# Kernel tuning notes

Hardware: AMD Instinct MI355X
Metric: run time of the kernel (lower is better)

## Reference

```python
import jax, jax.numpy as jnp
import numpy as np

NEG_SLOPE = 0.2  # PyG GATConv default negative_slope
N_NODES = 50000


def gat_conv(x, src, dst, W, att_src, att_dst, bias, heads, out_ch):
    # x: [N, F_in]; src/dst: [E] (messages flow src -> dst, softmax over dst)
    N = x.shape[0]
    h = (x @ W).reshape(N, heads, out_ch)              # [N,H,C]
    a_src = jnp.sum(h * att_src, axis=-1)              # [N,H]
    a_dst = jnp.sum(h * att_dst, axis=-1)              # [N,H]
    e = jax.nn.leaky_relu(a_src[src] + a_dst[dst], NEG_SLOPE)   # [E,H]
    # numerically stable segment softmax over incoming edges of each dst node
    m = jax.ops.segment_max(e, dst, num_segments=N)    # [N,H]
    e = jnp.exp(e - m[dst])
    denom = jax.ops.segment_sum(e, dst, num_segments=N)
    alpha = e / (denom[dst] + 1e-16)                   # [E,H]
    msg = h[src] * alpha[:, :, None]                   # [E,H,C]
    out = jax.ops.segment_sum(msg, dst, num_segments=N)  # [N,H,C]
    return out.reshape(N, heads * out_ch) + bias


def add_self_loops(edge_index, num_nodes):
    loop = jnp.arange(num_nodes, dtype=edge_index.dtype)
    return jnp.concatenate([edge_index, jnp.stack([loop, loop])], axis=1)


def setup_inputs() -> dict:
    key = jax.random.key(0)
    ks = jax.random.split(key, 10)
    F_in, H, C, F_out = 256, 4, 64, 16
    x = jax.random.normal(ks[0], (N_NODES, F_in), dtype=jnp.float32)
    edge_index = jax.random.randint(ks[1], (2, 800000), 0, N_NODES, dtype=jnp.int64)
    s1 = 1.0 / np.sqrt(F_in)
    s2 = 1.0 / np.sqrt(H * C)
    return {
        "x": x,
        "edge_index": edge_index,
        "W1": jax.random.normal(ks[2], (F_in, H * C), dtype=jnp.float32) * s1,
        "att_src1": jax.random.normal(ks[3], (H, C), dtype=jnp.float32) * s2,
        "att_dst1": jax.random.normal(ks[4], (H, C), dtype=jnp.float32) * s2,
        "b1": jnp.zeros((H * C,), dtype=jnp.float32),
        "W2": jax.random.normal(ks[5], (H * C, F_out), dtype=jnp.float32) * s2,
        "att_src2": jax.random.normal(ks[6], (1, F_out), dtype=jnp.float32) * 0.25,
        "att_dst2": jax.random.normal(ks[7], (1, F_out), dtype=jnp.float32) * 0.25,
        "b2": jnp.zeros((F_out,), dtype=jnp.float32),
    }


def reference(x, edge_index, W1, att_src1, att_dst1, b1, W2, att_src2, att_dst2, b2):
    ei = add_self_loops(edge_index, x.shape[0])
    src, dst = ei[0], ei[1]
    H1, C1 = att_src1.shape
    h = gat_conv(x, src, dst, W1, att_src1, att_dst1, b1, H1, C1)
    h = jax.nn.relu(h)
    # F.dropout(training=False) is identity in eval mode
    H2, C2 = att_src2.shape
    out = gat_conv(h, src, dst, W2, att_src2, att_dst2, b2, H2, C2)
    return jax.nn.log_softmax(out, axis=1)
```

## Files before the change

### kernel.cpp

```cpp
#include <hip/hip_runtime.h>
#include <math.h>


typedef __attribute__((ext_vector_type(8))) short bf16x8;
typedef __attribute__((ext_vector_type(8))) unsigned short u16x8;
typedef __attribute__((ext_vector_type(4))) float f32x4;
typedef __attribute__((ext_vector_type(2))) float f32x2;

static __device__ inline unsigned short f2bf(float f) {
    unsigned u = __builtin_bit_cast(unsigned, f);
    unsigned r = (u + 0x7FFF + ((u >> 16) & 1)) >> 16;
    return (unsigned short)r;
}
static __device__ inline float bf2f(unsigned short u) {
    unsigned v = ((unsigned)u) << 16;
    return __builtin_bit_cast(float, v);
}
static __device__ inline float lrelu(float x) { return x > 0.f ? x : 0.2f * x; }

__global__ __launch_bounds__(256) void k_prep(const float* __restrict__ W1,
                                              const float* __restrict__ b1,
                                              const float* __restrict__ W2,
                                              short* __restrict__ w1t,
                                              float* __restrict__ b1p,
                                              float* __restrict__ w2p,
                                              int* __restrict__ cnt,
                                              float* __restrict__ a1s,
                                              float* __restrict__ a2s,
                                              unsigned* __restrict__ h1f8u,
                                              float* __restrict__ h2,
                                              int N) {
    int idx = blockIdx.x * 256 + threadIdx.x;
    if (idx < N) cnt[idx] = 0;
    if (idx < 256) {
        int ct = (idx >> 6) * 64 + (idx & 3) * 16 + ((idx & 63) >> 2);
        b1p[idx] = b1[ct];
    }
    if (idx < 4096) {
        int pp = idx >> 4, c2 = idx & 15;
        int ct = (pp >> 6) * 64 + (pp & 3) * 16 + ((pp & 63) >> 2);
        w2p[idx] = W2[ct * 16 + c2];
    }
    if (idx < 4) a1s[(long)N * 4 + idx] = -1e30f;
    if (idx == 4) a2s[N] = -1e30f;
    if (idx < 64) h1f8u[(long)N * 64 + idx] = 0u;
    if (idx < 16) h2[(long)N * 16 + idx] = 0.f;
    int n = idx >> 8, k = idx & 255;
    w1t[n * 256 + k] = (short)f2bf(W1[k * 256 + n]);
}

__global__ __launch_bounds__(256) void k_scatter(const int* __restrict__ ei,
                                                 int* __restrict__ cnt,
                                                 int* __restrict__ csr,
                                                 int E0) {
    int e = blockIdx.x * 256 + threadIdx.x;
    if (e >= E0) return;
    int s = ei[e];
    int d = ei[E0 + e];
    int slot = atomicAdd(&cnt[d], 1);
    if (slot < 63) csr[((long)d << 6) + slot] = s << 4;
}

__global__ __launch_bounds__(256) void k_pad(const int* __restrict__ cnt,
                                             int* __restrict__ csr,
                                             int N) {
    int d = blockIdx.x * 256 + threadIdx.x;
    if (d >= N) return;
    int c = min(cnt[d], 63);
    long b = (long)d << 6;
    csr[b + c] = d << 4;
    int len4 = (c + 4) & ~3;
    for (int k = c + 1; k < len4; ++k) csr[b + k] = N << 4;
}

__global__ __launch_bounds__(256) void k_gemm1_mfma(const float* __restrict__ A,
                                                    const short* __restrict__ Bt,
                                                    const float* __restrict__ att_s,
                                                    const float* __restrict__ att_d,
                                                    unsigned char* __restrict__ C8,
                                                    float* __restrict__ a1s,
                                                    float* __restrict__ a1d,
                                                    int M) {
    __shared__ short As[128][40];
    __shared__ short Bs[128][40];
    const int bm = blockIdx.y * 128;
    const int bn = blockIdx.x * 128;
    const int tid = threadIdx.x;
    const int lane = tid & 63;
    const int wave = tid >> 6;
    const int wm = (wave >> 1) * 64;
    const int wn = (wave & 1) * 64;
    const int l15 = lane & 15;
    const int l4 = lane >> 4;

    const int sr = tid >> 1;
    const int sh = (tid & 1) * 16;

    f32x4 acc[4][4] = {};

    for (int k0 = 0; k0 < 256; k0 += 32) {
        {
            float v[16];
            if (bm + sr < M) {
                const float* p = &A[(long)(bm + sr) * 256 + k0 + sh];
#pragma unroll
                for (int q = 0; q < 4; ++q) {
                    float4 fv = *(const float4*)(p + q * 4);
                    v[q * 4 + 0] = fv.x; v[q * 4 + 1] = fv.y;
                    v[q * 4 + 2] = fv.z; v[q * 4 + 3] = fv.w;
                }
            } else {
#pragma unroll
                for (int q = 0; q < 16; ++q) v[q] = 0.f;
            }
            short b[16];
#pragma unroll
            for (int q = 0; q < 16; ++q) b[q] = (short)f2bf(v[q]);
            *(bf16x8*)&As[sr][sh] = *(bf16x8*)&b[0];
            *(bf16x8*)&As[sr][sh + 8] = *(bf16x8*)&b[8];
        }
        {
            const short* p = &Bt[(long)(bn + sr) * 256 + k0 + sh];
            bf16x8 b0 = *(const bf16x8*)p;
            bf16x8 b1 = *(const bf16x8*)(p + 8);
            *(bf16x8*)&Bs[sr][sh] = b0;
            *(bf16x8*)&Bs[sr][sh + 8] = b1;
        }
        __syncthreads();

        bf16x8 af[4], bfr[4];
#pragma unroll
        for (int i = 0; i < 4; ++i)
            af[i] = *(const bf16x8*)&As[wm + i * 16 + l15][l4 * 8];
#pragma unroll
        for (int j = 0; j < 4; ++j)
            bfr[j] = *(const bf16x8*)&Bs[wn + j * 16 + l15][l4 * 8];
#pragma unroll
        for (int i = 0; i < 4; ++i)
#pragma unroll
            for (int j = 0; j < 4; ++j)
                acc[i][j] = __builtin_amdgcn_mfma_f32_16x16x32_bf16(af[i], bfr[j], acc[i][j], 0, 0, 0);
        __syncthreads();
    }

    const int h = (bn + wn) >> 6;
    float aws[4], awd[4];
#pragma unroll
    for (int j = 0; j < 4; ++j) {
        aws[j] = att_s[h * 64 + j * 16 + l15];
        awd[j] = att_d[h * 64 + j * 16 + l15];
    }

#pragma unroll
    for (int i = 0; i < 4; ++i) {
#pragma unroll
        for (int r = 0; r < 4; ++r) {
            float sv = 0.f, dv = 0.f;
#pragma unroll
            for (int j = 0; j < 4; ++j) {
                sv += acc[i][j][r] * aws[j];
                dv += acc[i][j][r] * awd[j];
            }
#pragma unroll
            for (int o = 1; o < 16; o <<= 1) {
                sv += __shfl_xor(sv, o);
                dv += __shfl_xor(dv, o);
            }
            int row = bm + wm + i * 16 + l4 * 4 + r;
            if (row < M) {
                if (l15 == 0) { a1s[row * 4 + h] = sv; a1d[row * 4 + h] = dv; }
                int d = 0;
                d = __builtin_amdgcn_cvt_pk_fp8_f32(acc[i][0][r], acc[i][1][r], d, false);
                d = __builtin_amdgcn_cvt_pk_fp8_f32(acc[i][2][r], acc[i][3][r], d, true);
                *(unsigned*)&C8[(long)row * 256 + (bn + wn) + l15 * 4] = (unsigned)d;
            }
        }
    }
}

__global__ __launch_bounds__(256) void k_gather1(const unsigned char* __restrict__ h1f8,
                                                 const int* __restrict__ cnt,
                                                 const int* __restrict__ csr,
                                                 const float* __restrict__ as1,
                                                 const float* __restrict__ ad1,
                                                 const float* __restrict__ b1p,
                                                 unsigned short* __restrict__ out1b,
                                                 int N) {
    int wid = blockIdx.x * 4 + (threadIdx.x >> 6);
    int lane = threadIdx.x & 63;
    if (wid >= N) return;

    const int es = lane >> 4;
    const int cl = lane & 15;
    const int hc = cl >> 2;
    const float adh = ad1[wid * 4 + hc];

    int c = min(cnt[wid], 63);
    int len4 = (c + 4) & ~3;
    const int* seg = csr + ((long)wid << 6);
    const char* as1c = (const char*)as1 + hc * 4;
    const char* h1c  = (const char*)h1f8 + cl * 16;

    float dacc = 0.f;
    f32x2 acc2[8] = {};
#pragma unroll 2
    for (int j0 = 0; j0 < len4; j0 += 4) {
        int sv = seg[j0 + es];
        float a = __expf(lrelu(*(const float*)(as1c + sv) + adh));
        dacc += a;
        f32x2 av = {a, a};
        uint4 v = *(const uint4*)(h1c + ((long)sv << 4));
        unsigned w[4] = {v.x, v.y, v.z, v.w};
#pragma unroll
        for (int q = 0; q < 4; ++q) {
            f32x2 lo = __builtin_amdgcn_cvt_pk_f32_fp8((int)w[q], false);
            f32x2 hi = __builtin_amdgcn_cvt_pk_f32_fp8((int)w[q], true);
            acc2[q * 2 + 0] += av * lo;
            acc2[q * 2 + 1] += av * hi;
        }
    }
    dacc += __shfl_xor(dacc, 16);
    dacc += __shfl_xor(dacc, 32);
    const float inv_c = 1.f / (dacc + 1e-16f);

    float accf[16];
#pragma unroll
    for (int q = 0; q < 8; ++q) { accf[2 * q] = acc2[q].x; accf[2 * q + 1] = acc2[q].y; }
#pragma unroll
    for (int q = 0; q < 16; ++q) {
        accf[q] += __shfl_xor(accf[q], 16);
        accf[q] += __shfl_xor(accf[q], 32);
    }
    if (lane < 16) {
        unsigned pk[8];
#pragma unroll
        for (int q = 0; q < 8; ++q) {
            float v0 = fmaxf(accf[q * 2 + 0] * inv_c + b1p[cl * 16 + q * 2 + 0], 0.f);
            float v1 = fmaxf(accf[q * 2 + 1] * inv_c + b1p[cl * 16 + q * 2 + 1], 0.f);
            pk[q] = (unsigned)f2bf(v0) | ((unsigned)f2bf(v1) << 16);
        }
        unsigned short* dst = &out1b[(long)wid * 256 + cl * 16];
        *(uint4*)dst = make_uint4(pk[0], pk[1], pk[2], pk[3]);
        *(uint4*)(dst + 8) = make_uint4(pk[4], pk[5], pk[6], pk[7]);
    }
}

__global__ __launch_bounds__(256) void k_gemm2(const unsigned short* __restrict__ Xb,
                                               const float* __restrict__ Wp,
                                               const float* __restrict__ att_s,
                                               const float* __restrict__ att_d,
                                               float* __restrict__ h2,
                                               float* __restrict__ a2s,
                                               float* __restrict__ a2d, int N) {
    __shared__ float Ws[256 * 16];
    for (int i = threadIdx.x; i < 1024; i += 256)
        ((float4*)Ws)[i] = ((const float4*)Wp)[i];
    __syncthreads();
    int r = threadIdx.x >> 4, c = threadIdx.x & 15;
    int row = blockIdx.x * 16 + r;
    if (row >= N) return;
    const unsigned short* xr = Xb + (long)row * 256;
    float acc = 0.f;
    for (int k = 0; k < 256; k += 8) {
        u16x8 xv = *(const u16x8*)&xr[k];
#pragma unroll
        for (int q = 0; q < 8; ++q)
            acc += bf2f(xv[q]) * Ws[(k + q) * 16 + c];
    }
    h2[row * 16 + c] = acc;
    float vs = acc * att_s[c];
    float vd = acc * att_d[c];
    for (int o = 1; o < 16; o <<= 1) { vs += __shfl_xor(vs, o); vd += __shfl_xor(vd, o); }
    if (c == 0) { a2s[row] = vs; a2d[row] = vd; }
}

__global__ __launch_bounds__(256) void k_gather2(const float* __restrict__ h2,
                                                 const int* __restrict__ cnt,
                                                 const int* __restrict__ csr,
                                                 const float* __restrict__ a2s,
                                                 const float* __restrict__ a2d,
                                                 const float* __restrict__ b2,
                                                 float* __restrict__ out, int N) {
    int wid = blockIdx.x * 4 + (threadIdx.x >> 6);
    int lane = threadIdx.x & 63;
    if (wid >= N) return;
    float adh = a2d[wid];
    const int es = lane >> 4;
    const int c = lane & 15;

    int cc = min(cnt[wid], 63);
    int len4 = (cc + 4) & ~3;
    const int* seg = csr + ((long)wid << 6);
    const char* a2c = (const char*)a2s;
    const char* h2c = (const char*)h2 + c * 4;

    float dacc = 0.f;
    float acc = 0.f;
#pragma unroll 2
    for (int j0 = 0; j0 < len4; j0 += 4) {
        int sv = seg[j0 + es];
        float a = __expf(lrelu(*(const float*)(a2c + (sv >> 2)) + adh));
        dacc += a;
        acc += a * *(const float*)(h2c + (sv << 2));
    }
    acc += __shfl_xor(acc, 16);
    acc += __shfl_xor(acc, 32);
    dacc += __shfl_xor(dacc, 16);
    dacc += __shfl_xor(dacc, 32);
    float inv = 1.f / (dacc + 1e-16f);
    float v = acc * inv + b2[c];
    float mx = v;
    for (int o = 1; o < 16; o <<= 1) mx = fmaxf(mx, __shfl_xor(mx, o));
    float se = __expf(v - mx);
    for (int o = 1; o < 16; o <<= 1) se += __shfl_xor(se, o);
    float r = v - mx - logf(se);
    if (lane < 16) out[(long)wid * 16 + c] = r;
}

extern "C" void kernel_launch(void* const* d_in, const int* in_sizes, int n_in,
                              void* d_out, int out_size, void* d_ws, size_t ws_size,
                              hipStream_t stream) {
    const float* x    = (const float*)d_in[0];
    const int*   ei   = (const int*)d_in[1];
    const float* W1   = (const float*)d_in[2];
    const float* as1w = (const float*)d_in[3];
    const float* ad1w = (const float*)d_in[4];
    const float* b1   = (const float*)d_in[5];
    const float* W2   = (const float*)d_in[6];
    const float* as2w = (const float*)d_in[7];
    const float* ad2w = (const float*)d_in[8];
    const float* b2   = (const float*)d_in[9];
    float* out = (float*)d_out;

    const int N  = in_sizes[0] / 256;
    const int E0 = in_sizes[1] / 2;

    char* p = (char*)d_ws;
    unsigned char*  h1f8  = (unsigned char*)p;  p += (size_t)(N + 1) * 256;
    unsigned short* out1b = (unsigned short*)p; p += (size_t)N * 256 * sizeof(short);
    float* h2     = (float*)p; p += (size_t)(N + 1) * 16 * sizeof(float);
    float* a1s    = (float*)p; p += (size_t)(N + 1) * 4 * sizeof(float);
    float* a1d    = (float*)p; p += (size_t)N * 4 * sizeof(float);
    float* a2s    = (float*)p; p += (size_t)(N + 1) * sizeof(float);
    float* a2d    = (float*)p; p += (size_t)N * sizeof(float);
    float* b1p    = (float*)p; p += (size_t)256 * sizeof(float);
    float* w2p    = (float*)p; p += (size_t)4096 * sizeof(float);
    int*   cnt    = (int*)p;   p += (size_t)N * sizeof(int);
    short* w1t    = (short*)p; p += (size_t)256 * 256 * sizeof(short);
    int*   csr    = (int*)p;   p += (size_t)N * 64 * sizeof(int);

    const int NW = (N + 3) / 4;

    hipLaunchKernelGGL(k_prep, dim3(256), dim3(256), 0, stream,
                       W1, b1, W2, w1t, b1p, w2p, cnt, a1s, a2s,
                       (unsigned*)h1f8, h2, N);

    hipLaunchKernelGGL(k_scatter, dim3((E0 + 255) / 256), dim3(256), 0, stream,
                       ei, cnt, csr, E0);
    hipLaunchKernelGGL(k_pad, dim3((N + 255) / 256), dim3(256), 0, stream,
                       cnt, csr, N);

    hipLaunchKernelGGL(k_gemm1_mfma, dim3(2, (N + 127) / 128), dim3(256), 0, stream,
                       x, w1t, as1w, ad1w, h1f8, a1s, a1d, N);
    hipLaunchKernelGGL(k_gather1, dim3(NW), dim3(256), 0, stream,
                       h1f8, cnt, csr, a1s, a1d, b1p, out1b, N);

    hipLaunchKernelGGL(k_gemm2, dim3((N + 15) / 16), dim3(256), 0, stream,
                       out1b, w2p, as2w, ad2w, h2, a2s, a2d, N);
    hipLaunchKernelGGL(k_gather2, dim3(NW), dim3(256), 0, stream,
                       h2, cnt, csr, a2s, a2d, b2, out, N);
}
```

Measured before the change: 256.1 us.

## Merge edge scatter into GEMM1 launch as extra blocks to overlap them

Folds the CSR edge-scatter kernel into the first MFMA GEMM kernel by appending scatter blocks to a 1-D grid. GEMM tiles and atomic-heavy scatter work can then run concurrently on the GPU, and one launch is removed. Each scatter thread now handles 8 edges with vectorized int4 loads and batched atomics. The trade-offs are that k_pad now runs after the GEMM, and the heavyweight GEMM blocks share occupancy limits with the light scatter blocks.

Result: no change. 252.3 us (-1.5%).

```diff
diff --git a/kernel.cpp b/kernel.cpp
--- a/kernel.cpp
+++ b/kernel.cpp
@@ -49,18 +49,6 @@
     w1t[n * 256 + k] = (short)f2bf(W1[k * 256 + n]);
 }
 
-__global__ __launch_bounds__(256) void k_scatter(const int* __restrict__ ei,
-                                                 int* __restrict__ cnt,
-                                                 int* __restrict__ csr,
-                                                 int E0) {
-    int e = blockIdx.x * 256 + threadIdx.x;
-    if (e >= E0) return;
-    int s = ei[e];
-    int d = ei[E0 + e];
-    int slot = atomicAdd(&cnt[d], 1);
-    if (slot < 63) csr[((long)d << 6) + slot] = s << 4;
-}
-
 __global__ __launch_bounds__(256) void k_pad(const int* __restrict__ cnt,
                                              int* __restrict__ csr,
                                              int N) {
@@ -73,18 +61,49 @@
     for (int k = c + 1; k < len4; ++k) csr[b + k] = N << 4;
 }
 
-__global__ __launch_bounds__(256) void k_gemm1_mfma(const float* __restrict__ A,
-                                                    const short* __restrict__ Bt,
-                                                    const float* __restrict__ att_s,
-                                                    const float* __restrict__ att_d,
-                                                    unsigned char* __restrict__ C8,
-                                                    float* __restrict__ a1s,
-                                                    float* __restrict__ a1d,
-                                                    int M) {
+__global__ __launch_bounds__(256) void k_gemm1_scatter(
+        const float* __restrict__ A,
+        const short* __restrict__ Bt,
+        const float* __restrict__ att_s,
+        const float* __restrict__ att_d,
+        unsigned char* __restrict__ C8,
+        float* __restrict__ a1s,
+        float* __restrict__ a1d,
+        int M,
+        const int* __restrict__ ei,
+        int* __restrict__ cnt,
+        int* __restrict__ csr,
+        int E0, int GB) {
+    if ((int)blockIdx.x >= GB) {
+        int sb = (int)blockIdx.x - GB;
+        int e0 = sb * 2048 + ((int)threadIdx.x << 3);
+        if (e0 + 8 <= E0) {
+            int4 sa = *(const int4*)&ei[e0];
+            int4 sb4 = *(const int4*)&ei[e0 + 4];
+            int4 da = *(const int4*)&ei[E0 + e0];
+            int4 db = *(const int4*)&ei[E0 + e0 + 4];
+            int ss[8] = {sa.x, sa.y, sa.z, sa.w, sb4.x, sb4.y, sb4.z, sb4.w};
+            int dd[8] = {da.x, da.y, da.z, da.w, db.x, db.y, db.z, db.w};
+            int sl[8];
+#pragma unroll
+            for (int q = 0; q < 8; ++q) sl[q] = atomicAdd(&cnt[dd[q]], 1);
+#pragma unroll
+            for (int q = 0; q < 8; ++q)
+                if (sl[q] < 63) csr[((long)dd[q] << 6) + sl[q]] = ss[q] << 4;
+        } else {
+            for (int e = e0; e < E0; ++e) {
+                int s = ei[e], d = ei[E0 + e];
+                int slot = atomicAdd(&cnt[d], 1);
+                if (slot < 63) csr[((long)d << 6) + slot] = s << 4;
+            }
+        }
+        return;
+    }
+
     __shared__ short As[128][40];
     __shared__ short Bs[128][40];
-    const int bm = blockIdx.y * 128;
-    const int bn = blockIdx.x * 128;
+    const int bm = ((int)blockIdx.x >> 1) * 128;
+    const int bn = ((int)blockIdx.x & 1) * 128;
     const int tid = threadIdx.x;
     const int lane = tid & 63;
     const int wave = tid >> 6;
@@ -355,13 +374,14 @@
                        W1, b1, W2, w1t, b1p, w2p, cnt, a1s, a2s,
                        (unsigned*)h1f8, h2, N);
 
-    hipLaunchKernelGGL(k_scatter, dim3((E0 + 255) / 256), dim3(256), 0, stream,
-                       ei, cnt, csr, E0);
+    const int GB = 2 * ((N + 127) / 128);
+    const int SB = (E0 + 2047) / 2048;
+    hipLaunchKernelGGL(k_gemm1_scatter, dim3(GB + SB), dim3(256), 0, stream,
+                       x, w1t, as1w, ad1w, h1f8, a1s, a1d, N,
+                       ei, cnt, csr, E0, GB);
     hipLaunchKernelGGL(k_pad, dim3((N + 255) / 256), dim3(256), 0, stream,
                        cnt, csr, N);
 
-    hipLaunchKernelGGL(k_gemm1_mfma, dim3(2, (N + 127) / 128), dim3(256), 0, stream,
-                       x, w1t, as1w, ad1w, h1f8, a1s, a1d, N);
     hipLaunchKernelGGL(k_gather1, dim3(NW), dim3(256), 0, stream,
                        h1f8, cnt, csr, a1s, a1d, b1p, out1b, N);
 
```

## Fold x bf16 conversion and CSR self-loop init into prep, drop pad kernel

Applied to the files above, without the earlier changes.

The prep kernel now converts x to bf16 into a reused workspace buffer and pre-fills the whole CSR with the self-loop in slot 0 plus sentinel padding, with counts starting at 1. This removes the separate pad kernel. Scatter handles four edges per thread with vectorized loads, and gemm1 reads bf16 A directly with smaller 64-row M tiles so there are more blocks. The trade-off is that prep now writes the full 50000x64 CSR and an extra bf16 copy of x, so it moves more memory. The self-loop also moves from the end of each neighbour list to the front.

New measurement: 263.8 us. +3.0%, slower.

```diff
diff --git a/kernel.cpp b/kernel.cpp
--- a/kernel.cpp
+++ b/kernel.cpp
@@ -18,9 +18,12 @@
 }
 static __device__ inline float lrelu(float x) { return x > 0.f ? x : 0.2f * x; }
 
-__global__ __launch_bounds__(256) void k_prep(const float* __restrict__ W1,
+__global__ __launch_bounds__(256) void k_prep(const float* __restrict__ x,
+                                              const float* __restrict__ W1,
                                               const float* __restrict__ b1,
                                               const float* __restrict__ W2,
+                                              short* __restrict__ xb,
+                                              int* __restrict__ csr,
                                               short* __restrict__ w1t,
                                               float* __restrict__ b1p,
                                               float* __restrict__ w2p,
@@ -30,14 +33,30 @@
                                               unsigned* __restrict__ h1f8u,
                                               float* __restrict__ h2,
                                               int N) {
-    int idx = blockIdx.x * 256 + threadIdx.x;
-    if (idx < N) cnt[idx] = 0;
+    long idx = (long)blockIdx.x * 256 + threadIdx.x;
+    const long T = (long)N * 32;
+    if (idx < T) {
+        const float* xp = x + idx * 8;
+        float4 f0 = *(const float4*)xp;
+        float4 f1 = *(const float4*)(xp + 4);
+        short b[8];
+        b[0] = (short)f2bf(f0.x); b[1] = (short)f2bf(f0.y);
+        b[2] = (short)f2bf(f0.z); b[3] = (short)f2bf(f0.w);
+        b[4] = (short)f2bf(f1.x); b[5] = (short)f2bf(f1.y);
+        b[6] = (short)f2bf(f1.z); b[7] = (short)f2bf(f1.w);
+        *(bf16x8*)(xb + idx * 8) = *(bf16x8*)&b[0];
+        long p = idx * 2;
+        int v0 = ((p & 63) == 0) ? (int)((p >> 6) << 4) : (N << 4);
+        int v1 = N << 4;
+        *(int2*)(csr + p) = make_int2(v0, v1);
+    }
+    if (idx < N) cnt[idx] = 1;
     if (idx < 256) {
-        int ct = (idx >> 6) * 64 + (idx & 3) * 16 + ((idx & 63) >> 2);
+        int ct = ((int)idx >> 6) * 64 + ((int)idx & 3) * 16 + (((int)idx & 63) >> 2);
         b1p[idx] = b1[ct];
     }
     if (idx < 4096) {
-        int pp = idx >> 4, c2 = idx & 15;
+        int pp = (int)idx >> 4, c2 = (int)idx & 15;
         int ct = (pp >> 6) * 64 + (pp & 3) * 16 + ((pp & 63) >> 2);
         w2p[idx] = W2[ct * 16 + c2];
     }
@@ -45,35 +64,39 @@
     if (idx == 4) a2s[N] = -1e30f;
     if (idx < 64) h1f8u[(long)N * 64 + idx] = 0u;
     if (idx < 16) h2[(long)N * 16 + idx] = 0.f;
-    int n = idx >> 8, k = idx & 255;
-    w1t[n * 256 + k] = (short)f2bf(W1[k * 256 + n]);
+    if (idx < 65536) {
+        int n = (int)idx >> 8, k = (int)idx & 255;
+        w1t[n * 256 + k] = (short)f2bf(W1[k * 256 + n]);
+    }
 }
 
 __global__ __launch_bounds__(256) void k_scatter(const int* __restrict__ ei,
                                                  int* __restrict__ cnt,
                                                  int* __restrict__ csr,
                                                  int E0) {
-    int e = blockIdx.x * 256 + threadIdx.x;
-    if (e >= E0) return;
-    int s = ei[e];
-    int d = ei[E0 + e];
-    int slot = atomicAdd(&cnt[d], 1);
-    if (slot < 63) csr[((long)d << 6) + slot] = s << 4;
-}
-
-__global__ __launch_bounds__(256) void k_pad(const int* __restrict__ cnt,
-                                             int* __restrict__ csr,
-                                             int N) {
-    int d = blockIdx.x * 256 + threadIdx.x;
-    if (d >= N) return;
-    int c = min(cnt[d], 63);
-    long b = (long)d << 6;
-    csr[b + c] = d << 4;
-    int len4 = (c + 4) & ~3;
-    for (int k = c + 1; k < len4; ++k) csr[b + k] = N << 4;
-}
-
-__global__ __launch_bounds__(256) void k_gemm1_mfma(const float* __restrict__ A,
+    int e0 = (blockIdx.x * 256 + threadIdx.x) << 2;
+    if (e0 >= E0) return;
+    if (e0 + 4 <= E0) {
+        int4 s4 = *(const int4*)&ei[e0];
+        int4 d4 = *(const int4*)&ei[E0 + e0];
+        int ss[4] = {s4.x, s4.y, s4.z, s4.w};
+        int dd[4] = {d4.x, d4.y, d4.z, d4.w};
+        int sl[4];
+#pragma unroll
+        for (int q = 0; q < 4; ++q) sl[q] = atomicAdd(&cnt[dd[q]], 1);
+#pragma unroll
+        for (int q = 0; q < 4; ++q)
+            if (sl[q] < 64) csr[((long)dd[q] << 6) + sl[q]] = ss[q] << 4;
+    } else {
+        for (int e = e0; e < E0; ++e) {
+            int s = ei[e], d = ei[E0 + e];
+            int slot = atomicAdd(&cnt[d], 1);
+            if (slot < 64) csr[((long)d << 6) + slot] = s << 4;
+        }
+    }
+}
+
+__global__ __launch_bounds__(256) void k_gemm1_mfma(const short* __restrict__ Ab,
                                                     const short* __restrict__ Bt,
                                                     const float* __restrict__ att_s,
                                                     const float* __restrict__ att_d,
@@ -81,62 +104,48 @@
                                                     float* __restrict__ a1s,
                                                     float* __restrict__ a1d,
                                                     int M) {
-    __shared__ short As[128][40];
+    __shared__ short As[64][40];
     __shared__ short Bs[128][40];
-    const int bm = blockIdx.y * 128;
+    const int bm = blockIdx.y * 64;
     const int bn = blockIdx.x * 128;
     const int tid = threadIdx.x;
     const int lane = tid & 63;
     const int wave = tid >> 6;
-    const int wm = (wave >> 1) * 64;
+    const int wm = (wave >> 1) * 32;
     const int wn = (wave & 1) * 64;
     const int l15 = lane & 15;
     const int l4 = lane >> 4;
 
-    const int sr = tid >> 1;
-    const int sh = (tid & 1) * 16;
-
-    f32x4 acc[4][4] = {};
+    const int ar = tid >> 2, aq = (tid & 3) * 8;
+    const int br = tid >> 1, bh = (tid & 1) * 16;
+
+    f32x4 acc[2][4] = {};
 
     for (int k0 = 0; k0 < 256; k0 += 32) {
         {
-            float v[16];
-            if (bm + sr < M) {
-                const float* p = &A[(long)(bm + sr) * 256 + k0 + sh];
-#pragma unroll
-                for (int q = 0; q < 4; ++q) {
-                    float4 fv = *(const float4*)(p + q * 4);
-                    v[q * 4 + 0] = fv.x; v[q * 4 + 1] = fv.y;
-                    v[q * 4 + 2] = fv.z; v[q * 4 + 3] = fv.w;
-                }
+            bf16x8 av;
+            if (bm + ar < M) {
+                av = *(const bf16x8*)&Ab[(long)(bm + ar) * 256 + k0 + aq];
             } else {
 #pragma unroll
-                for (int q = 0; q < 16; ++q) v[q] = 0.f;
+                for (int q = 0; q < 8; ++q) av[q] = 0;
             }
-            short b[16];
-#pragma unroll
-            for (int q = 0; q < 16; ++q) b[q] = (short)f2bf(v[q]);
-            *(bf16x8*)&As[sr][sh] = *(bf16x8*)&b[0];
-            *(bf16x8*)&As[sr][sh + 8] = *(bf16x8*)&b[8];
-        }
-        {
-            const short* p = &Bt[(long)(bn + sr) * 256 + k0 + sh];
-            bf16x8 b0 = *(const bf16x8*)p;
-            bf16x8 b1 = *(const bf16x8*)(p + 8);
-            *(bf16x8*)&Bs[sr][sh] = b0;
-            *(bf16x8*)&Bs[sr][sh + 8] = b1;
+            *(bf16x8*)&As[ar][aq] = av;
+            const short* p = &Bt[(long)(bn + br) * 256 + k0 + bh];
+            *(bf16x8*)&Bs[br][bh] = *(const bf16x8*)p;
+            *(bf16x8*)&Bs[br][bh + 8] = *(const bf16x8*)(p + 8);
         }
         __syncthreads();
 
-        bf16x8 af[4], bfr[4];
-#pragma unroll
-        for (int i = 0; i < 4; ++i)
+        bf16x8 af[2], bfr[4];
+#pragma unroll
+        for (int i = 0; i < 2; ++i)
             af[i] = *(const bf16x8*)&As[wm + i * 16 + l15][l4 * 8];
 #pragma unroll
         for (int j = 0; j < 4; ++j)
             bfr[j] = *(const bf16x8*)&Bs[wn + j * 16 + l15][l4 * 8];
 #pragma unroll
-        for (int i = 0; i < 4; ++i)
+        for (int i = 0; i < 2; ++i)
 #pragma unroll
             for (int j = 0; j < 4; ++j)
                 acc[i][j] = __builtin_amdgcn_mfma_f32_16x16x32_bf16(af[i], bfr[j], acc[i][j], 0, 0, 0);
@@ -152,7 +161,7 @@
     }
 
 #pragma unroll
-    for (int i = 0; i < 4; ++i) {
+    for (int i = 0; i < 2; ++i) {
 #pragma unroll
         for (int r = 0; r < 4; ++r) {
             float sv = 0.f, dv = 0.f;
@@ -195,8 +204,8 @@
     const int hc = cl >> 2;
     const float adh = ad1[wid * 4 + hc];
 
-    int c = min(cnt[wid], 63);
-    int len4 = (c + 4) & ~3;
+    int c = min(cnt[wid], 64);
+    int len4 = (c + 3) & ~3;
     const int* seg = csr + ((long)wid << 6);
     const char* as1c = (const char*)as1 + hc * 4;
     const char* h1c  = (const char*)h1f8 + cl * 16;
@@ -288,8 +297,8 @@
     const int es = lane >> 4;
     const int c = lane & 15;
 
-    int cc = min(cnt[wid], 63);
-    int len4 = (cc + 4) & ~3;
+    int cc = min(cnt[wid], 64);
+    int len4 = (cc + 3) & ~3;
     const int* seg = csr + ((long)wid << 6);
     const char* a2c = (const char*)a2s;
     const char* h2c = (const char*)h2 + c * 4;
@@ -349,19 +358,21 @@
     short* w1t    = (short*)p; p += (size_t)256 * 256 * sizeof(short);
     int*   csr    = (int*)p;   p += (size_t)N * 64 * sizeof(int);
 
+    short* xb = (short*)out1b;
+
     const int NW = (N + 3) / 4;
 
-    hipLaunchKernelGGL(k_prep, dim3(256), dim3(256), 0, stream,
-                       W1, b1, W2, w1t, b1p, w2p, cnt, a1s, a2s,
+    const long T = (long)N * 32;
+    hipLaunchKernelGGL(k_prep, dim3((unsigned)((T + 255) / 256)), dim3(256), 0, stream,
+                       x, W1, b1, W2, xb, csr, w1t, b1p, w2p, cnt, a1s, a2s,
                        (unsigned*)h1f8, h2, N);
 
-    hipLaunchKernelGGL(k_scatter, dim3((E0 + 255) / 256), dim3(256), 0, stream,
+    const int E4 = (E0 + 3) / 4;
+    hipLaunchKernelGGL(k_scatter, dim3((E4 + 255) / 256), dim3(256), 0, stream,
                        ei, cnt, csr, E0);
-    hipLaunchKernelGGL(k_pad, dim3((N + 255) / 256), dim3(256), 0, stream,
-                       cnt, csr, N);
-
-    hipLaunchKernelGGL(k_gemm1_mfma, dim3(2, (N + 127) / 128), dim3(256), 0, stream,
-                       x, w1t, as1w, ad1w, h1f8, a1s, a1d, N);
+
+    hipLaunchKernelGGL(k_gemm1_mfma, dim3(2, (N + 63) / 64), dim3(256), 0, stream,
+                       xb, w1t, as1w, ad1w, h1f8, a1s, a1d, N);
     hipLaunchKernelGGL(k_gather1, dim3(NW), dim3(256), 0, stream,
                        h1f8, cnt, csr, a1s, a1d, b1p, out1b, N);
 
```
